# Performance work log

Measured on AMD Instinct MI355X. Metric: run time of the kernel, lower is better.

## Reference

```python
import jax, jax.numpy as jnp
import numpy as np

B, T, D, H = 8, 1024, 768, 12
HD = D // H  # head_dim = 64


def setup_inputs() -> dict:
    key = jax.random.key(0)
    ks = jax.random.split(key, 6)
    s = 1.0 / np.sqrt(D)
    return {
        "x": jax.random.normal(ks[0], (B, T, D), dtype=jnp.float32),
        "Wq": jax.random.normal(ks[1], (D, D), dtype=jnp.float32) * s,
        "Wk": jax.random.normal(ks[2], (D, D), dtype=jnp.float32) * s,
        "Wv": jax.random.normal(ks[3], (D, D), dtype=jnp.float32) * s,
        "Wp": jax.random.normal(ks[4], (D, D), dtype=jnp.float32) * s,
        "bp": jnp.zeros((D,), dtype=jnp.float32),
    }


def reference(x, Wq, Wk, Wv, Wp, bp):
    Bx, Tx, Dx = x.shape
    # projections (nn.Linear applies x @ W.T; weights here are stored as [out,in]-equivalent square)
    q = (x @ Wq.T).reshape(Bx, Tx, H, HD).transpose(0, 2, 1, 3)  # [B,H,T,hd]
    k = (x @ Wk.T).reshape(Bx, Tx, H, HD).transpose(0, 2, 1, 3)
    v = (x @ Wv.T).reshape(Bx, Tx, H, HD).transpose(0, 2, 1, 3)
    scores = jnp.einsum("bhqd,bhkd->bhqk", q, k)  # raw QK^T, then mask, then scale (as in source)
    causal = jnp.tril(jnp.ones((Tx, Tx), dtype=bool))
    scores = jnp.where(causal, scores, -jnp.inf)
    weights = jax.nn.softmax(scores / np.sqrt(HD), axis=-1)
    # dropout is identity in eval mode
    ctx = jnp.einsum("bhqk,bhkd->bhqd", weights, v)
    ctx = ctx.transpose(0, 2, 1, 3).reshape(Bx, Tx, Dx)
    return ctx @ Wp.T + bp
```

## Files before the change

### kernel.cpp

```cpp
#include <hip/hip_runtime.h>
#include <math.h>

#define Bsz 8
#define Tsz 1024
#define Dsz 768
#define Hn  12
#define Msz (Bsz*Tsz)
#define NQT (Tsz/64)

typedef __attribute__((ext_vector_type(8))) short bf16x8_t;
typedef __attribute__((ext_vector_type(4))) float f32x4_t;

__device__ __forceinline__ unsigned short f2bf(float f) {
  unsigned u = __builtin_bit_cast(unsigned, f);
  u += 0x7FFFu + ((u >> 16) & 1u);
  return (unsigned short)(u >> 16);
}

__device__ __forceinline__ void gload16(const void* g, const void* l) {
  __builtin_amdgcn_global_load_lds(
      (const __attribute__((address_space(1))) unsigned int*)g,
      (__attribute__((address_space(3))) unsigned int*)l, 16, 0, 0);
}

__global__ __launch_bounds__(256) void cvt_x_kernel(const float* __restrict__ in,
                                                    unsigned short* __restrict__ out) {
  size_t idx = ((size_t)blockIdx.x * 256 + threadIdx.x) * 4;
  float4 v = *(const float4*)(in + idx);
  union { unsigned short u[4]; uint2 w; } t;
  t.u[0] = f2bf(v.x); t.u[1] = f2bf(v.y); t.u[2] = f2bf(v.z); t.u[3] = f2bf(v.w);
  *(uint2*)(out + idx) = t.w;
}

__global__ __launch_bounds__(256) void cvt_w_kernel(
    const float* __restrict__ w0, const float* __restrict__ w1,
    const float* __restrict__ w2, const float* __restrict__ w3,
    unsigned short* __restrict__ o0, unsigned short* __restrict__ o1,
    unsigned short* __restrict__ o2, unsigned short* __restrict__ o3) {
  const float* src; unsigned short* dst;
  switch (blockIdx.y) {
    case 0: src = w0; dst = o0; break;
    case 1: src = w1; dst = o1; break;
    case 2: src = w2; dst = o2; break;
    default: src = w3; dst = o3; break;
  }
  size_t idx = ((size_t)blockIdx.x * 256 + threadIdx.x) * 4;
  float4 v = *(const float4*)(src + idx);
  union { unsigned short u[4]; uint2 w; } t;
  t.u[0] = f2bf(v.x); t.u[1] = f2bf(v.y); t.u[2] = f2bf(v.z); t.u[3] = f2bf(v.w);
  *(uint2*)(dst + idx) = t.w;
}

__global__ __launch_bounds__(256) void gemm_qkv_kernel(
    const unsigned short* __restrict__ X, const unsigned short* __restrict__ Wcat,
    unsigned short* __restrict__ Yq, unsigned short* __restrict__ Yk,
    unsigned short* __restrict__ Yvt) {
  __shared__ __align__(16) unsigned short As[128 * 32];
  __shared__ __align__(16) unsigned short Bs[128 * 32];
  const int tid = threadIdx.x;
  const int w = tid >> 6, lane = tid & 63;
  const int i = lane & 15, g = lane >> 4;
  const int wr = w >> 1, wc = w & 1;
  const int bm = blockIdx.x * 128, bn = blockIdx.y * 128;

  f32x4_t acc[4][4];
  #pragma unroll
  for (int a = 0; a < 4; ++a)
    #pragma unroll
    for (int b2 = 0; b2 < 4; ++b2)
      #pragma unroll
      for (int r = 0; r < 4; ++r) acc[a][b2][r] = 0.f;

  for (int k0 = 0; k0 < Dsz; k0 += 32) {
    __syncthreads();
    #pragma unroll
    for (int j = 0; j < 2; ++j) {
      const int c = 2 * w + j;
      const int row = 16 * c + (lane >> 2);
      const int cb = (lane & 3) * 16;
      const char* ga = (const char*)X + ((size_t)(bm + row) * Dsz + k0) * 2 + cb;
      gload16(ga, (const char*)As + c * 1024);
      const char* gb = (const char*)Wcat + ((size_t)(bn + row) * Dsz + k0) * 2 + cb;
      gload16(gb, (const char*)Bs + c * 1024);
    }
    __syncthreads();
    bf16x8_t af[4], bfr[4];
    #pragma unroll
    for (int f = 0; f < 4; ++f) {
      af[f]  = *(const bf16x8_t*)&As[(64 * wr + 16 * f + i) * 32 + 8 * g];
      bfr[f] = *(const bf16x8_t*)&Bs[(64 * wc + 16 * f + i) * 32 + 8 * g];
    }
    #pragma unroll
    for (int a = 0; a < 4; ++a)
      #pragma unroll
      for (int b2 = 0; b2 < 4; ++b2)
        acc[a][b2] = __builtin_amdgcn_mfma_f32_16x16x32_bf16(af[a], bfr[b2], acc[a][b2], 0, 0, 0);
  }

  const int wsel = blockIdx.y / 6;
  const int nloc = (blockIdx.y % 6) * 128;
  if (wsel < 2) {
    unsigned short* Y = wsel ? Yk : Yq;
    const float sc = wsel ? 1.0f : 0.18033688f;
    #pragma unroll
    for (int fi = 0; fi < 4; ++fi)
      #pragma unroll
      for (int fj = 0; fj < 4; ++fj) {
        const int n = nloc + 64 * wc + 16 * fj + i;
        #pragma unroll
        for (int r = 0; r < 4; ++r) {
          const int m = bm + 64 * wr + 16 * fi + 4 * g + r;
          Y[(size_t)m * Dsz + n] = f2bf(acc[fi][fj][r] * sc);
        }
      }
  } else {
    #pragma unroll
    for (int fi = 0; fi < 4; ++fi)
      #pragma unroll
      for (int fj = 0; fj < 4; ++fj) {
        const int m0 = bm + 64 * wr + 16 * fi + 4 * g;
        const int bb = m0 >> 10;
        const int t  = m0 & 1023;
        const int n  = nloc + 64 * wc + 16 * fj + i;
        union { unsigned short u[4]; uint2 v; } pk;
        #pragma unroll
        for (int r = 0; r < 4; ++r) pk.u[r] = f2bf(acc[fi][fj][r]);
        *(uint2*)&Yvt[((size_t)(bb * Dsz + n)) * Tsz + t] = pk.v;
      }
  }
}

__global__ __launch_bounds__(256) void gemm_proj_kernel(
    const unsigned short* __restrict__ X, const unsigned short* __restrict__ W,
    const float* __restrict__ bias, float* __restrict__ Y) {
  __shared__ __align__(16) unsigned short As[128 * 32];
  __shared__ __align__(16) unsigned short Bs[128 * 32];
  const int tid = threadIdx.x;
  const int w = tid >> 6, lane = tid & 63;
  const int i = lane & 15, g = lane >> 4;
  const int wr = w >> 1, wc = w & 1;
  const int bm = blockIdx.x * 128, bn = blockIdx.y * 128;

  f32x4_t acc[4][4];
  #pragma unroll
  for (int a = 0; a < 4; ++a)
    #pragma unroll
    for (int b2 = 0; b2 < 4; ++b2)
      #pragma unroll
      for (int r = 0; r < 4; ++r) acc[a][b2][r] = 0.f;

  for (int k0 = 0; k0 < Dsz; k0 += 32) {
    __syncthreads();
    #pragma unroll
    for (int j = 0; j < 2; ++j) {
      const int c = 2 * w + j;
      const int row = 16 * c + (lane >> 2);
      const int cb = (lane & 3) * 16;
      const char* ga = (const char*)X + ((size_t)(bm + row) * Dsz + k0) * 2 + cb;
      gload16(ga, (const char*)As + c * 1024);
      const char* gb = (const char*)W + ((size_t)(bn + row) * Dsz + k0) * 2 + cb;
      gload16(gb, (const char*)Bs + c * 1024);
    }
    __syncthreads();
    bf16x8_t af[4], bfr[4];
    #pragma unroll
    for (int f = 0; f < 4; ++f) {
      af[f]  = *(const bf16x8_t*)&As[(64 * wr + 16 * f + i) * 32 + 8 * g];
      bfr[f] = *(const bf16x8_t*)&Bs[(64 * wc + 16 * f + i) * 32 + 8 * g];
    }
    #pragma unroll
    for (int a = 0; a < 4; ++a)
      #pragma unroll
      for (int b2 = 0; b2 < 4; ++b2)
        acc[a][b2] = __builtin_amdgcn_mfma_f32_16x16x32_bf16(af[a], bfr[b2], acc[a][b2], 0, 0, 0);
  }

  #pragma unroll
  for (int fi = 0; fi < 4; ++fi)
    #pragma unroll
    for (int fj = 0; fj < 4; ++fj) {
      const int n = bn + 64 * wc + 16 * fj + i;
      const float bv = bias[n];
      #pragma unroll
      for (int r = 0; r < 4; ++r) {
        const int m = bm + 64 * wr + 16 * fi + 4 * g + r;
        Y[(size_t)m * Dsz + n] = acc[fi][fj][r] + bv;
      }
    }
}

__global__ __launch_bounds__(256) void attn_mfma_kernel(
    const unsigned short* __restrict__ Qm, const unsigned short* __restrict__ Km,
    const unsigned short* __restrict__ Vt, unsigned short* __restrict__ ctx) {
  __shared__ __align__(16) unsigned short KP[4 * 16 * 136];
  __shared__ __align__(16) unsigned short Vs[64 * 128];
  unsigned short* Ks = KP;
  const int tid = threadIdx.x, w = tid >> 6, lane = tid & 63;
  const int i = lane & 15, g = lane >> 4;
  const int bh = blockIdx.y, b = bh / Hn, h = bh % Hn;
  const int kr8 = lane >> 3;
  const int kb8 = (lane & 7) * 16;
  const int vr4 = lane >> 4;
  const int vb4 = (lane & 15) * 16;

  for (int tsel = 0; tsel < 2; ++tsel) {
    const int qt = tsel ? (NQT - 1 - (int)blockIdx.x) : (int)blockIdx.x;
    const int t0 = qt * 64;

    bf16x8_t qa[2];
    {
      const unsigned short* qp =
          Qm + ((size_t)(b * Tsz + t0 + 16 * w + i) * Dsz + h * 64 + 8 * g);
      qa[0] = *(const bf16x8_t*)qp;
      qa[1] = *(const bf16x8_t*)(qp + 32);
    }

    f32x4_t o[4];
    #pragma unroll
    for (int fd = 0; fd < 4; ++fd)
      #pragma unroll
      for (int r = 0; r < 4; ++r) o[fd][r] = 0.f;
    float mrun[4] = {-3.0e38f, -3.0e38f, -3.0e38f, -3.0e38f};
    float lrun[4] = {0.f, 0.f, 0.f, 0.f};

    const int nt2 = qt / 2 + 1;
    for (int kt2 = 0; kt2 < nt2; ++kt2) {
      const int k0 = kt2 * 128;
      const bool uh = (k0 + 64) <= (t0 + 63);
      const int nfj = uh ? 8 : 4;
      const int nks = uh ? 4 : 2;
      const bool dtile = (kt2 == (qt >> 1));

      __syncthreads();
      #pragma unroll
      for (int j = 0; j < 4; ++j) {
        const int c = 4 * j + w;
        const int krow = 8 * c + kr8;
        const char* gk = (const char*)Km +
            ((size_t)(b * Tsz + k0 + krow) * Dsz + h * 64) * 2 +
            (kb8 ^ ((kr8 & 7) << 4));
        gload16(gk, (const char*)Ks + c * 1024);
        const int vrow = 4 * c + vr4;
        const char* gv = (const char*)Vt +
            ((size_t)(bh * 64 + vrow) * Tsz + k0) * 2 +
            (vb4 ^ ((vrow & 7) << 4));
        gload16(gv, (const char*)Vs + c * 1024);
      }
      __syncthreads();

      f32x4_t s[8];
      #pragma unroll
      for (int fj = 0; fj < 8; ++fj) {
        if (fj >= nfj) continue;
        #pragma unroll
        for (int r = 0; r < 4; ++r) s[fj][r] = 0.f;
        #pragma unroll
        for (int ks = 0; ks < 2; ++ks) {
          const int R = 16 * fj + i;
          const bf16x8_t kb = *(const bf16x8_t*)((const char*)Ks + R * 128 +
                                                 ((16 * g + 64 * ks) ^ ((R & 7) << 4)));
          s[fj] = __builtin_amdgcn_mfma_f32_16x16x32_bf16(qa[ks], kb, s[fj], 0, 0, 0);
        }
      }

      if (dtile) {
        #pragma unroll
        for (int fj = 0; fj < 8; ++fj) {
          if (fj >= nfj) continue;
          const int kidx = k0 + 16 * fj + i;
          #pragma unroll
          for (int r = 0; r < 4; ++r)
            if (kidx > t0 + 16 * w + 4 * g + r) s[fj][r] = -1.0e30f;
        }
      }

      float mx[4] = {-3.0e38f, -3.0e38f, -3.0e38f, -3.0e38f};
      #pragma unroll
      for (int fj = 0; fj < 8; ++fj) {
        if (fj >= nfj) continue;
        #pragma unroll
        for (int r = 0; r < 4; ++r) mx[r] = fmaxf(mx[r], s[fj][r]);
      }
      #pragma unroll
      for (int r = 0; r < 4; ++r) {
        mx[r] = fmaxf(mx[r], __shfl_xor(mx[r], 1));
        mx[r] = fmaxf(mx[r], __shfl_xor(mx[r], 2));
        mx[r] = fmaxf(mx[r], __shfl_xor(mx[r], 4));
        mx[r] = fmaxf(mx[r], __shfl_xor(mx[r], 8));
      }

      bool nd = false;
      #pragma unroll
      for (int r = 0; r < 4; ++r) nd = nd || (mx[r] > mrun[r] + 8.0f);
      if (__any(nd)) {
        #pragma unroll
        for (int r = 0; r < 4; ++r) {
          const float mn = fmaxf(mrun[r], mx[r]);
          const float fs = exp2f(mrun[r] - mn);
          mrun[r] = mn;
          lrun[r] *= fs;
          #pragma unroll
          for (int fd = 0; fd < 4; ++fd) o[fd][r] *= fs;
        }
      }

      float rs[4] = {0.f, 0.f, 0.f, 0.f};
      #pragma unroll
      for (int fj = 0; fj < 8; ++fj) {
        if (fj >= nfj) continue;
        #pragma unroll
        for (int r = 0; r < 4; ++r) {
          s[fj][r] = exp2f(s[fj][r] - mrun[r]);
          rs[r] += s[fj][r];
        }
      }
      #pragma unroll
      for (int r = 0; r < 4; ++r) {
        rs[r] += __shfl_xor(rs[r], 1);
        rs[r] += __shfl_xor(rs[r], 2);
        rs[r] += __shfl_xor(rs[r], 4);
        rs[r] += __shfl_xor(rs[r], 8);
        lrun[r] += rs[r];
      }

      __syncthreads();

      unsigned short* Pw = KP + w * (16 * 136);
      #pragma unroll
      for (int fj = 0; fj < 8; ++fj) {
        if (fj >= nfj) continue;
        #pragma unroll
        for (int r = 0; r < 4; ++r)
          Pw[(4 * g + r) * 136 + 16 * fj + i] = f2bf(s[fj][r]);
      }

      #pragma unroll
      for (int ks = 0; ks < 4; ++ks) {
        if (ks >= nks) continue;
        const bf16x8_t pa = *(const bf16x8_t*)&Pw[i * 136 + 32 * ks + 8 * g];
        #pragma unroll
        for (int fd = 0; fd < 4; ++fd) {
          const int R = 16 * fd + i;
          const bf16x8_t vb = *(const bf16x8_t*)((const char*)Vs + R * 256 +
                                                 ((16 * g + 64 * ks) ^ ((R & 7) << 4)));
          o[fd] = __builtin_amdgcn_mfma_f32_16x16x32_bf16(pa, vb, o[fd], 0, 0, 0);
        }
      }
    }

    #pragma unroll
    for (int r = 0; r < 4; ++r) {
      const float inv = 1.f / lrun[r];
      const int qidx = t0 + 16 * w + 4 * g + r;
      #pragma unroll
      for (int fd = 0; fd < 4; ++fd)
        ctx[(size_t)(b * Tsz + qidx) * Dsz + h * 64 + 16 * fd + i] =
            f2bf(o[fd][r] * inv);
    }
  }
}

extern "C" void kernel_launch(void* const* d_in, const int* in_sizes, int n_in,
                              void* d_out, int out_size, void* d_ws, size_t ws_size,
                              hipStream_t stream) {
  const float* x  = (const float*)d_in[0];
  const float* Wq = (const float*)d_in[1];
  const float* Wk = (const float*)d_in[2];
  const float* Wv = (const float*)d_in[3];
  const float* Wp = (const float*)d_in[4];
  const float* bp = (const float*)d_in[5];
  float* out = (float*)d_out;

  const size_t md = (size_t)Msz * Dsz;
  const size_t wd = (size_t)Dsz * Dsz;
  unsigned short* xb   = (unsigned short*)d_ws;
  unsigned short* wqb  = xb + md;
  unsigned short* wkb  = wqb + wd;
  unsigned short* wvb  = wkb + wd;
  unsigned short* wpb  = wvb + wd;
  unsigned short* qb   = wpb + wd;
  unsigned short* kb   = qb + md;
  unsigned short* vtb  = kb + md;
  unsigned short* ctxb = vtb + md;

  cvt_x_kernel<<<md / 1024, 256, 0, stream>>>(x, xb);
  cvt_w_kernel<<<dim3(wd / 1024, 4), 256, 0, stream>>>(Wq, Wk, Wv, Wp, wqb, wkb, wvb, wpb);

  gemm_qkv_kernel<<<dim3(Msz / 128, 18), 256, 0, stream>>>(xb, wqb, qb, kb, vtb);

  attn_mfma_kernel<<<dim3(NQT / 2, Bsz * Hn), 256, 0, stream>>>(qb, kb, vtb, ctxb);

  gemm_proj_kernel<<<dim3(Msz / 128, Dsz / 128), 256, 0, stream>>>(ctxb, wpb, bp, out);
}
```

Before: 228.9 us.

## Double-buffer attention KV tiles into one fused loop and merge conversion kernels

Restructures the attention kernel to walk 64-wide KV tiles for both of its query tiles in one flattened loop. The next K/V tile is prefetched into a second LDS buffer while the current one is computed, which removes one barrier per iteration and hides load latency. MFMA sections are raised with s_setprio. The two fp32-to-bf16 conversion kernels are merged into a single launch, and the manual rounding is replaced by the library bf16 conversion. Smaller tiles mean more iterations and more softmax-reduction overhead per key, and the library conversion may differ in NaN handling.

```diff
diff --git a/kernel.cpp b/kernel.cpp
--- a/kernel.cpp
+++ b/kernel.cpp
@@ -1,4 +1,5 @@
 #include <hip/hip_runtime.h>
+#include <hip/hip_bf16.h>
 #include <math.h>
 
 #define Bsz 8
@@ -17,34 +18,41 @@
   return (unsigned short)(u >> 16);
 }
 
+__device__ __forceinline__ unsigned short f2bf_fast(float f) {
+  __hip_bfloat16 h = __float2bfloat16(f);
+  return __builtin_bit_cast(unsigned short, h);
+}
+
 __device__ __forceinline__ void gload16(const void* g, const void* l) {
   __builtin_amdgcn_global_load_lds(
       (const __attribute__((address_space(1))) unsigned int*)g,
       (__attribute__((address_space(3))) unsigned int*)l, 16, 0, 0);
 }
 
-__global__ __launch_bounds__(256) void cvt_x_kernel(const float* __restrict__ in,
-                                                    unsigned short* __restrict__ out) {
-  size_t idx = ((size_t)blockIdx.x * 256 + threadIdx.x) * 4;
-  float4 v = *(const float4*)(in + idx);
-  union { unsigned short u[4]; uint2 w; } t;
-  t.u[0] = f2bf(v.x); t.u[1] = f2bf(v.y); t.u[2] = f2bf(v.z); t.u[3] = f2bf(v.w);
-  *(uint2*)(out + idx) = t.w;
-}
-
-__global__ __launch_bounds__(256) void cvt_w_kernel(
+#define XBLKS (Msz*Dsz/1024)
+#define WBLKS (Dsz*Dsz/1024)
+__global__ __launch_bounds__(256) void cvt_all_kernel(
+    const float* __restrict__ x,
     const float* __restrict__ w0, const float* __restrict__ w1,
     const float* __restrict__ w2, const float* __restrict__ w3,
+    unsigned short* __restrict__ xb,
     unsigned short* __restrict__ o0, unsigned short* __restrict__ o1,
     unsigned short* __restrict__ o2, unsigned short* __restrict__ o3) {
-  const float* src; unsigned short* dst;
-  switch (blockIdx.y) {
-    case 0: src = w0; dst = o0; break;
-    case 1: src = w1; dst = o1; break;
-    case 2: src = w2; dst = o2; break;
-    default: src = w3; dst = o3; break;
-  }
-  size_t idx = ((size_t)blockIdx.x * 256 + threadIdx.x) * 4;
+  int bid = blockIdx.x;
+  const float* src; unsigned short* dst; size_t blk;
+  if (bid < XBLKS) { src = x; dst = xb; blk = bid; }
+  else {
+    int t = bid - XBLKS;
+    int which = t / WBLKS;
+    blk = t % WBLKS;
+    switch (which) {
+      case 0: src = w0; dst = o0; break;
+      case 1: src = w1; dst = o1; break;
+      case 2: src = w2; dst = o2; break;
+      default: src = w3; dst = o3; break;
+    }
+  }
+  size_t idx = (blk * 256 + threadIdx.x) * 4;
   float4 v = *(const float4*)(src + idx);
   union { unsigned short u[4]; uint2 w; } t;
   t.u[0] = f2bf(v.x); t.u[1] = f2bf(v.y); t.u[2] = f2bf(v.z); t.u[3] = f2bf(v.w);
@@ -78,10 +86,10 @@
       const int c = 2 * w + j;
       const int row = 16 * c + (lane >> 2);
       const int cb = (lane & 3) * 16;
-      const char* ga = (const char*)X + ((size_t)(bm + row) * Dsz + k0) * 2 + cb;
-      gload16(ga, (const char*)As + c * 1024);
-      const char* gb = (const char*)Wcat + ((size_t)(bn + row) * Dsz + k0) * 2 + cb;
-      gload16(gb, (const char*)Bs + c * 1024);
+      gload16((const char*)X + ((size_t)(bm + row) * Dsz + k0) * 2 + cb,
+              (const char*)As + c * 1024);
+      gload16((const char*)Wcat + ((size_t)(bn + row) * Dsz + k0) * 2 + cb,
+              (const char*)Bs + c * 1024);
     }
     __syncthreads();
     bf16x8_t af[4], bfr[4];
@@ -110,7 +118,7 @@
         #pragma unroll
         for (int r = 0; r < 4; ++r) {
           const int m = bm + 64 * wr + 16 * fi + 4 * g + r;
-          Y[(size_t)m * Dsz + n] = f2bf(acc[fi][fj][r] * sc);
+          Y[(size_t)m * Dsz + n] = f2bf_fast(acc[fi][fj][r] * sc);
         }
       }
   } else {
@@ -124,7 +132,7 @@
         const int n  = nloc + 64 * wc + 16 * fj + i;
         union { unsigned short u[4]; uint2 v; } pk;
         #pragma unroll
-        for (int r = 0; r < 4; ++r) pk.u[r] = f2bf(acc[fi][fj][r]);
+        for (int r = 0; r < 4; ++r) pk.u[r] = f2bf_fast(acc[fi][fj][r]);
         *(uint2*)&Yvt[((size_t)(bb * Dsz + n)) * Tsz + t] = pk.v;
       }
   }
@@ -156,10 +164,10 @@
       const int c = 2 * w + j;
       const int row = 16 * c + (lane >> 2);
       const int cb = (lane & 3) * 16;
-      const char* ga = (const char*)X + ((size_t)(bm + row) * Dsz + k0) * 2 + cb;
-      gload16(ga, (const char*)As + c * 1024);
-      const char* gb = (const char*)W + ((size_t)(bn + row) * Dsz + k0) * 2 + cb;
-      gload16(gb, (const char*)Bs + c * 1024);
+      gload16((const char*)X + ((size_t)(bm + row) * Dsz + k0) * 2 + cb,
+              (const char*)As + c * 1024);
+      gload16((const char*)W + ((size_t)(bn + row) * Dsz + k0) * 2 + cb,
+              (const char*)Bs + c * 1024);
     }
     __syncthreads();
     bf16x8_t af[4], bfr[4];
@@ -192,162 +200,178 @@
 __global__ __launch_bounds__(256) void attn_mfma_kernel(
     const unsigned short* __restrict__ Qm, const unsigned short* __restrict__ Km,
     const unsigned short* __restrict__ Vt, unsigned short* __restrict__ ctx) {
-  __shared__ __align__(16) unsigned short KP[4 * 16 * 136];
-  __shared__ __align__(16) unsigned short Vs[64 * 128];
-  unsigned short* Ks = KP;
+  __shared__ __align__(16) unsigned short Ks[2][64 * 64];
+  __shared__ __align__(16) unsigned short Vs[2][64 * 64];
+  __shared__ __align__(16) unsigned short Ps[4][16 * 72];
   const int tid = threadIdx.x, w = tid >> 6, lane = tid & 63;
   const int i = lane & 15, g = lane >> 4;
   const int bh = blockIdx.y, b = bh / Hn, h = bh % Hn;
-  const int kr8 = lane >> 3;
-  const int kb8 = (lane & 7) * 16;
-  const int vr4 = lane >> 4;
-  const int vb4 = (lane & 15) * 16;
-
-  for (int tsel = 0; tsel < 2; ++tsel) {
-    const int qt = tsel ? (NQT - 1 - (int)blockIdx.x) : (int)blockIdx.x;
+  const int qtA = blockIdx.x, qtB = NQT - 1 - qtA;
+  const int ntot = qtA + qtB + 2;
+
+  const int sr  = lane >> 3;
+  const int swz = ((lane & 7) * 16) ^ (sr << 4);
+
+  bf16x8_t qa[2][2];
+  #pragma unroll
+  for (int ts = 0; ts < 2; ++ts) {
+    const int t0 = (ts ? qtB : qtA) * 64;
+    const unsigned short* qp =
+        Qm + ((size_t)(b * Tsz + t0 + 16 * w + i) * Dsz + h * 64 + 8 * g);
+    qa[ts][0] = *(const bf16x8_t*)qp;
+    qa[ts][1] = *(const bf16x8_t*)(qp + 32);
+  }
+
+  f32x4_t o[4];
+  #pragma unroll
+  for (int fd = 0; fd < 4; ++fd)
+    #pragma unroll
+    for (int r = 0; r < 4; ++r) o[fd][r] = 0.f;
+  float mrun[4] = {-3.0e38f, -3.0e38f, -3.0e38f, -3.0e38f};
+  float lrun[4] = {0.f, 0.f, 0.f, 0.f};
+
+  auto STAGE = [&](int kv0, int p) {
+    #pragma unroll
+    for (int j = 0; j < 2; ++j) {
+      const int c = 2 * w + j;
+      const int row = 8 * c + sr;
+      gload16((const char*)Km + ((size_t)(b * Tsz + kv0 + row) * Dsz + h * 64) * 2 + swz,
+              (const char*)Ks[p] + c * 1024);
+      gload16((const char*)Vt + ((size_t)(bh * 64 + row) * Tsz + kv0) * 2 + swz,
+              (const char*)Vs[p] + c * 1024);
+    }
+  };
+
+  STAGE(0, 0);
+
+  unsigned short* Pw = &Ps[w][0];
+
+  for (int fi = 0; fi < ntot; ++fi) {
+    const int p = fi & 1;
+    const int ts = (fi > qtA) ? 1 : 0;
+    const int qt = ts ? qtB : qtA;
     const int t0 = qt * 64;
-
-    bf16x8_t qa[2];
-    {
-      const unsigned short* qp =
-          Qm + ((size_t)(b * Tsz + t0 + 16 * w + i) * Dsz + h * 64 + 8 * g);
-      qa[0] = *(const bf16x8_t*)qp;
-      qa[1] = *(const bf16x8_t*)(qp + 32);
-    }
-
-    f32x4_t o[4];
-    #pragma unroll
-    for (int fd = 0; fd < 4; ++fd)
-      #pragma unroll
-      for (int r = 0; r < 4; ++r) o[fd][r] = 0.f;
-    float mrun[4] = {-3.0e38f, -3.0e38f, -3.0e38f, -3.0e38f};
-    float lrun[4] = {0.f, 0.f, 0.f, 0.f};
-
-    const int nt2 = qt / 2 + 1;
-    for (int kt2 = 0; kt2 < nt2; ++kt2) {
-      const int k0 = kt2 * 128;
-      const bool uh = (k0 + 64) <= (t0 + 63);
-      const int nfj = uh ? 8 : 4;
-      const int nks = uh ? 4 : 2;
-      const bool dtile = (kt2 == (qt >> 1));
-
-      __syncthreads();
-      #pragma unroll
-      for (int j = 0; j < 4; ++j) {
-        const int c = 4 * j + w;
-        const int krow = 8 * c + kr8;
-        const char* gk = (const char*)Km +
-            ((size_t)(b * Tsz + k0 + krow) * Dsz + h * 64) * 2 +
-            (kb8 ^ ((kr8 & 7) << 4));
-        gload16(gk, (const char*)Ks + c * 1024);
-        const int vrow = 4 * c + vr4;
-        const char* gv = (const char*)Vt +
-            ((size_t)(bh * 64 + vrow) * Tsz + k0) * 2 +
-            (vb4 ^ ((vrow & 7) << 4));
-        gload16(gv, (const char*)Vs + c * 1024);
-      }
-      __syncthreads();
-
-      f32x4_t s[8];
-      #pragma unroll
-      for (int fj = 0; fj < 8; ++fj) {
-        if (fj >= nfj) continue;
-        #pragma unroll
-        for (int r = 0; r < 4; ++r) s[fj][r] = 0.f;
-        #pragma unroll
-        for (int ks = 0; ks < 2; ++ks) {
-          const int R = 16 * fj + i;
-          const bf16x8_t kb = *(const bf16x8_t*)((const char*)Ks + R * 128 +
-                                                 ((16 * g + 64 * ks) ^ ((R & 7) << 4)));
-          s[fj] = __builtin_amdgcn_mfma_f32_16x16x32_bf16(qa[ks], kb, s[fj], 0, 0, 0);
-        }
-      }
-
-      if (dtile) {
-        #pragma unroll
-        for (int fj = 0; fj < 8; ++fj) {
-          if (fj >= nfj) continue;
-          const int kidx = k0 + 16 * fj + i;
-          #pragma unroll
-          for (int r = 0; r < 4; ++r)
-            if (kidx > t0 + 16 * w + 4 * g + r) s[fj][r] = -1.0e30f;
-        }
-      }
-
-      float mx[4] = {-3.0e38f, -3.0e38f, -3.0e38f, -3.0e38f};
-      #pragma unroll
-      for (int fj = 0; fj < 8; ++fj) {
-        if (fj >= nfj) continue;
-        #pragma unroll
-        for (int r = 0; r < 4; ++r) mx[r] = fmaxf(mx[r], s[fj][r]);
-      }
+    const int kt = ts ? (fi - qtA - 1) : fi;
+
+    __syncthreads();
+
+    if (fi + 1 < ntot) {
+      const int nf = fi + 1;
+      const int nkt = (nf > qtA) ? (nf - qtA - 1) : nf;
+      STAGE(nkt * 64, p ^ 1);
+    }
+
+    f32x4_t s[4];
+    __builtin_amdgcn_s_setprio(1);
+    #pragma unroll
+    for (int fj = 0; fj < 4; ++fj) {
+      #pragma unroll
+      for (int r = 0; r < 4; ++r) s[fj][r] = 0.f;
+      const int R = 16 * fj + i;
+      #pragma unroll
+      for (int ks = 0; ks < 2; ++ks) {
+        const bf16x8_t kb = *(const bf16x8_t*)((const char*)Ks[p] + R * 128 +
+                                               ((64 * ks + 16 * g) ^ ((i & 7) << 4)));
+        s[fj] = __builtin_amdgcn_mfma_f32_16x16x32_bf16(qa[ts][ks], kb, s[fj], 0, 0, 0);
+      }
+    }
+    __builtin_amdgcn_s_setprio(0);
+
+    if (kt == qt) {
+      #pragma unroll
+      for (int fj = 0; fj < 4; ++fj) {
+        const int kidx = kt * 64 + 16 * fj + i;
+        #pragma unroll
+        for (int r = 0; r < 4; ++r)
+          if (kidx > t0 + 16 * w + 4 * g + r) s[fj][r] = -1.0e30f;
+      }
+    }
+
+    float mx[4];
+    #pragma unroll
+    for (int r = 0; r < 4; ++r)
+      mx[r] = fmaxf(fmaxf(s[0][r], s[1][r]), fmaxf(s[2][r], s[3][r]));
+    #pragma unroll
+    for (int r = 0; r < 4; ++r) {
+      mx[r] = fmaxf(mx[r], __shfl_xor(mx[r], 1));
+      mx[r] = fmaxf(mx[r], __shfl_xor(mx[r], 2));
+      mx[r] = fmaxf(mx[r], __shfl_xor(mx[r], 4));
+      mx[r] = fmaxf(mx[r], __shfl_xor(mx[r], 8));
+    }
+
+    bool nd = false;
+    #pragma unroll
+    for (int r = 0; r < 4; ++r) nd = nd || (mx[r] > mrun[r] + 8.0f);
+    if (__any(nd)) {
       #pragma unroll
       for (int r = 0; r < 4; ++r) {
-        mx[r] = fmaxf(mx[r], __shfl_xor(mx[r], 1));
-        mx[r] = fmaxf(mx[r], __shfl_xor(mx[r], 2));
-        mx[r] = fmaxf(mx[r], __shfl_xor(mx[r], 4));
-        mx[r] = fmaxf(mx[r], __shfl_xor(mx[r], 8));
-      }
-
-      bool nd = false;
-      #pragma unroll
-      for (int r = 0; r < 4; ++r) nd = nd || (mx[r] > mrun[r] + 8.0f);
-      if (__any(nd)) {
-        #pragma unroll
-        for (int r = 0; r < 4; ++r) {
-          const float mn = fmaxf(mrun[r], mx[r]);
-          const float fs = exp2f(mrun[r] - mn);
-          mrun[r] = mn;
-          lrun[r] *= fs;
-          #pragma unroll
-          for (int fd = 0; fd < 4; ++fd) o[fd][r] *= fs;
-        }
-      }
-
-      float rs[4] = {0.f, 0.f, 0.f, 0.f};
-      #pragma unroll
-      for (int fj = 0; fj < 8; ++fj) {
-        if (fj >= nfj) continue;
-        #pragma unroll
-        for (int r = 0; r < 4; ++r) {
-          s[fj][r] = exp2f(s[fj][r] - mrun[r]);
-          rs[r] += s[fj][r];
-        }
-      }
+        const float mn = fmaxf(mrun[r], mx[r]);
+        const float fs = exp2f(mrun[r] - mn);
+        mrun[r] = mn;
+        lrun[r] *= fs;
+        #pragma unroll
+        for (int fd = 0; fd < 4; ++fd) o[fd][r] *= fs;
+      }
+    }
+
+    float rs[4] = {0.f, 0.f, 0.f, 0.f};
+    #pragma unroll
+    for (int fj = 0; fj < 4; ++fj)
       #pragma unroll
       for (int r = 0; r < 4; ++r) {
-        rs[r] += __shfl_xor(rs[r], 1);
-        rs[r] += __shfl_xor(rs[r], 2);
-        rs[r] += __shfl_xor(rs[r], 4);
-        rs[r] += __shfl_xor(rs[r], 8);
-        lrun[r] += rs[r];
-      }
-
-      __syncthreads();
-
-      unsigned short* Pw = KP + w * (16 * 136);
-      #pragma unroll
-      for (int fj = 0; fj < 8; ++fj) {
-        if (fj >= nfj) continue;
-        #pragma unroll
-        for (int r = 0; r < 4; ++r)
-          Pw[(4 * g + r) * 136 + 16 * fj + i] = f2bf(s[fj][r]);
-      }
-
-      #pragma unroll
-      for (int ks = 0; ks < 4; ++ks) {
-        if (ks >= nks) continue;
-        const bf16x8_t pa = *(const bf16x8_t*)&Pw[i * 136 + 32 * ks + 8 * g];
-        #pragma unroll
-        for (int fd = 0; fd < 4; ++fd) {
-          const int R = 16 * fd + i;
-          const bf16x8_t vb = *(const bf16x8_t*)((const char*)Vs + R * 256 +
-                                                 ((16 * g + 64 * ks) ^ ((R & 7) << 4)));
-          o[fd] = __builtin_amdgcn_mfma_f32_16x16x32_bf16(pa, vb, o[fd], 0, 0, 0);
-        }
-      }
-    }
-
+        s[fj][r] = exp2f(s[fj][r] - mrun[r]);
+        rs[r] += s[fj][r];
+      }
+    #pragma unroll
+    for (int r = 0; r < 4; ++r) {
+      rs[r] += __shfl_xor(rs[r], 1);
+      rs[r] += __shfl_xor(rs[r], 2);
+      rs[r] += __shfl_xor(rs[r], 4);
+      rs[r] += __shfl_xor(rs[r], 8);
+      lrun[r] += rs[r];
+    }
+
+    #pragma unroll
+    for (int fj = 0; fj < 4; ++fj)
+      #pragma unroll
+      for (int r = 0; r < 4; ++r)
+        Pw[(4 * g + r) * 72 + 16 * fj + i] = f2bf_fast(s[fj][r]);
+
+    __builtin_amdgcn_s_setprio(1);
+    #pragma unroll
+    for (int ks = 0; ks < 2; ++ks) {
+      const bf16x8_t pa = *(const bf16x8_t*)&Pw[i * 72 + 32 * ks + 8 * g];
+      #pragma unroll
+      for (int fd = 0; fd < 4; ++fd) {
+        const int R = 16 * fd + i;
+        const bf16x8_t vb = *(const bf16x8_t*)((const char*)Vs[p] + R * 128 +
+                                               ((64 * ks + 16 * g) ^ ((i & 7) << 4)));
+        o[fd] = __builtin_amdgcn_mfma_f32_16x16x32_bf16(pa, vb, o[fd], 0, 0, 0);
+      }
+    }
+    __builtin_amdgcn_s_setprio(0);
+
+    if (fi == qtA) {
+      #pragma unroll
+      for (int r = 0; r < 4; ++r) {
+        const float inv = 1.f / lrun[r];
+        const int qidx = t0 + 16 * w + 4 * g + r;
+        #pragma unroll
+        for (int fd = 0; fd < 4; ++fd)
+          ctx[(size_t)(b * Tsz + qidx) * Dsz + h * 64 + 16 * fd + i] =
+              f2bf_fast(o[fd][r] * inv);
+      }
+      #pragma unroll
+      for (int fd = 0; fd < 4; ++fd)
+        #pragma unroll
+        for (int r = 0; r < 4; ++r) o[fd][r] = 0.f;
+      #pragma unroll
+      for (int r = 0; r < 4; ++r) { mrun[r] = -3.0e38f; lrun[r] = 0.f; }
+    }
+  }
+
+  {
+    const int t0 = qtB * 64;
     #pragma unroll
     for (int r = 0; r < 4; ++r) {
       const float inv = 1.f / lrun[r];
@@ -355,7 +379,7 @@
       #pragma unroll
       for (int fd = 0; fd < 4; ++fd)
         ctx[(size_t)(b * Tsz + qidx) * Dsz + h * 64 + 16 * fd + i] =
-            f2bf(o[fd][r] * inv);
+            f2bf_fast(o[fd][r] * inv);
     }
   }
 }
@@ -383,8 +407,8 @@
   unsigned short* vtb  = kb + md;
   unsigned short* ctxb = vtb + md;
 
-  cvt_x_kernel<<<md / 1024, 256, 0, stream>>>(x, xb);
-  cvt_w_kernel<<<dim3(wd / 1024, 4), 256, 0, stream>>>(Wq, Wk, Wv, Wp, wqb, wkb, wvb, wpb);
+  cvt_all_kernel<<<XBLKS + 4 * WBLKS, 256, 0, stream>>>(
+      x, Wq, Wk, Wv, Wp, xb, wqb, wkb, wvb, wpb);
 
   gemm_qkv_kernel<<<dim3(Msz / 128, 18), 256, 0, stream>>>(xb, wqb, qb, kb, vtb);
 
```

After: 206.5 us. 9.8% less time.
